# Optimization experiments

Hardware: AMD Instinct MI355X
Metric: run time of the kernel (lower is better)

Reference implementation:

```python
import jax, jax.numpy as jnp
import numpy as np

B, N, E, M, H = 2, 4096, 65536, 4, 256


def setup_inputs() -> dict:
    key = jax.random.key(0)
    ks = jax.random.split(key, 8)
    src = jax.random.randint(ks[0], (B, E), 0, N, dtype=jnp.int32)
    # targets: permutation of arange(E) % N per batch -> every node has >=1 incoming edge
    base = jnp.arange(E, dtype=jnp.int32) % N
    tgt = jnp.stack([jax.random.permutation(jax.random.fold_in(ks[1], b), base) for b in range(B)], axis=0)
    cfg_indices_padded = jnp.stack([src, tgt], axis=-1)  # [B, E, 2]
    hint_state = jax.random.normal(ks[2], (B, N, M, H), dtype=jnp.float32)
    node_fts = jax.random.normal(ks[3], (B, N, M, H), dtype=jnp.float32)
    edge_fts = jax.random.normal(ks[4], (B, E, H), dtype=jnp.float32)
    # hk.Linear default init scales
    edge_W = jax.random.truncated_normal(ks[5], -2.0, 2.0, (H, 1), dtype=jnp.float32) / np.sqrt(H)
    edge_b = jnp.zeros((1,), dtype=jnp.float32)
    update_W = jax.random.truncated_normal(ks[6], -2.0, 2.0, (H, H), dtype=jnp.float32) / np.sqrt(H)
    update_b = jnp.zeros((H,), dtype=jnp.float32)
    return {
        'cfg_indices_padded': cfg_indices_padded,
        'hint_state': hint_state,
        'node_fts': node_fts,
        'edge_fts': edge_fts,
        'edge_W': edge_W,
        'edge_b': edge_b,
        'update_W': update_W,
        'update_b': update_b,
    }


def reference(cfg_indices_padded, hint_state, node_fts, edge_fts, edge_W, edge_b, update_W, update_b):
    nb_nodes = node_fts.shape[1]
    src = cfg_indices_padded[..., 0]  # [B, E]
    tgt = cfg_indices_padded[..., 1]  # [B, E]
    # gather hint states at edge sources: [B, E, M, H]
    hint_sources = jnp.take_along_axis(hint_state, src[:, :, None, None], axis=1)
    # learned per-edge scalar coefficient: [B, E, 1]
    edge_coeff = edge_fts @ edge_W + edge_b
    hint_sources = edge_coeff[..., None] * hint_sources  # [B, E, M, H]
    # segment_max scatter-reduce per batch element -> [B, N, M, H]
    seg_max = jax.vmap(lambda d, s: jax.ops.segment_max(d, s, num_segments=nb_nodes))
    aggregated_hint = seg_max(hint_sources, tgt)
    # final linear update
    return (node_fts + aggregated_hint) @ update_W + update_b
```

## Files before the change

### kernel.cpp

```cpp
#include <hip/hip_runtime.h>

#define BB 2
#define NN 4096
#define EE 65536
#define MM 4
#define HH 256
#define NPB 16
#define NXCD 8
#define XPAD 264

typedef float vf4 __attribute__((ext_vector_type(4)));
typedef int vi2 __attribute__((ext_vector_type(2)));
typedef _Float16 vh4 __attribute__((ext_vector_type(4)));
typedef _Float16 f16x8 __attribute__((ext_vector_type(8)));
typedef float f32x4 __attribute__((ext_vector_type(4)));

#define PREP_A 2048
#define PREP_B 8192
#define PREP_C 64

__global__ __launch_bounds__(256) void k_prep(const float* __restrict__ edge_fts,
                                              const float* __restrict__ edge_W,
                                              const float* __restrict__ edge_b,
                                              const int* __restrict__ cfg,
                                              unsigned int* __restrict__ cnt,
                                              int2* __restrict__ packed,
                                              const float* __restrict__ hint,
                                              _Float16* __restrict__ h16,
                                              const float* __restrict__ W,
                                              _Float16* __restrict__ wt_hi) {
  const int blk = blockIdx.x;
  const int t = threadIdx.x;
  if (blk < PREP_A) {
    const int e0 = blk * 64 + (t >> 6) * 16;
    const int lane = t & 63;
    const float4 wv = *reinterpret_cast<const float4*>(edge_W + lane * 4);
    float s[16];
#pragma unroll
    for (int q = 0; q < 16; ++q) {
      const vf4 ef = __builtin_nontemporal_load(
          reinterpret_cast<const vf4*>(edge_fts + (size_t)(e0 + q) * HH + lane * 4));
      s[q] = ef.x * wv.x + ef.y * wv.y + ef.z * wv.z + ef.w * wv.w;
    }
#pragma unroll
    for (int off = 1; off < 64; off <<= 1) {
#pragma unroll
      for (int q = 0; q < 16; ++q) s[q] += __shfl_xor(s[q], off);
    }
    if (lane < 16) {
      float sv = s[15];
#pragma unroll
      for (int q = 14; q >= 0; --q) sv = (lane == q) ? s[q] : sv;
      const int widx = e0 + lane;
      const int b = widx >> 16;
      const vi2 st = __builtin_nontemporal_load(
          reinterpret_cast<const vi2*>(cfg + (size_t)widx * 2));
      const int slot = b * NN + st.y;
      const unsigned p = atomicAdd(&cnt[slot], 1u) & 15u;
      int2 v;
      v.x = st.x;
      v.y = __float_as_int(sv + edge_b[0]);
      packed[(size_t)slot * 16 + p] = v;
    }
  } else if (blk < PREP_A + PREP_B) {
    const int j = blk - PREP_A;
    const int unit = j & 7;
    const int g = j >> 3;
    const int b = unit >> 2;
    const int m = unit & 3;
    const int row = g * 4 + (t >> 6);
    const int c4 = t & 63;
    const size_t off = (((size_t)(b * NN + row) * MM + m) * HH) + c4 * 4;
    const vf4 v = __builtin_nontemporal_load(
        reinterpret_cast<const vf4*>(hint + off));
    vh4 h;
    h.x = (_Float16)v.x; h.y = (_Float16)v.y;
    h.z = (_Float16)v.z; h.w = (_Float16)v.w;
    *reinterpret_cast<vh4*>(h16 + off) = h;
  } else {
    const int jb = blk - PREP_A - PREP_B;
    const int j = jb * 4 + (t >> 6);
    const int h0 = (t & 63) * 4;
    vh4 hi;
    hi.x = (_Float16)W[(size_t)(h0 + 0) * HH + j];
    hi.y = (_Float16)W[(size_t)(h0 + 1) * HH + j];
    hi.z = (_Float16)W[(size_t)(h0 + 2) * HH + j];
    hi.w = (_Float16)W[(size_t)(h0 + 3) * HH + j];
    *reinterpret_cast<vh4*>(wt_hi + (size_t)j * HH + h0) = hi;
  }
}

__device__ __forceinline__ float4 fmax4(const float4& a, const float4& b) {
  return make_float4(fmaxf(a.x, b.x), fmaxf(a.y, b.y), fmaxf(a.z, b.z), fmaxf(a.w, b.w));
}

__device__ __forceinline__ float4 scmul(float c, const vh4& h) {
  return make_float4(c * (float)h.x, c * (float)h.y, c * (float)h.z, c * (float)h.w);
}

__global__ __launch_bounds__(256, 6) void k_fused(const _Float16* __restrict__ h16,
                                                  const float* __restrict__ node_fts,
                                                  const int2* __restrict__ packed,
                                                  const _Float16* __restrict__ wt_hi,
                                                  const float* __restrict__ bias,
                                                  float* __restrict__ out) {
  __shared__ _Float16 xs[NPB][XPAD];
  __shared__ int ssrc[NPB][16];
  __shared__ float scf[NPB][16];

  const int t = threadIdx.x;
  const int unit = blockIdx.x & (NXCD - 1);
  const int chunk = blockIdx.x >> 3;
  const int b = unit >> 2;
  const int m = unit & 3;
  const int n0 = chunk * NPB;
  const int w = t >> 6;
  const int lane = t & 63;
  const int r0 = w * 4;

  {
    const int i = t >> 4, k = t & 15;
    const int2 v = packed[(size_t)(b * NN + n0 + i) * 16 + k];
    ssrc[i][k] = v.x;
    scf[i][k] = __int_as_float(v.y);
  }

  const _Float16* hb = h16 + (size_t)b * NN * MM * HH + m * HH + lane * 4;

#pragma unroll 1
  for (int i = 0; i < 4; ++i) {
    const int lr = r0 + i;
    const int n = n0 + lr;
    vh4 hv[16];
#pragma unroll
    for (int k = 0; k < 16; ++k) {
      const int s = ssrc[lr][k];
      hv[k] = *reinterpret_cast<const vh4*>(hb + (size_t)s * (MM * HH));
    }
    float4 t8[8];
#pragma unroll
    for (int k = 0; k < 8; ++k)
      t8[k] = fmax4(scmul(scf[lr][2 * k], hv[2 * k]),
                    scmul(scf[lr][2 * k + 1], hv[2 * k + 1]));
#pragma unroll
    for (int k = 0; k < 4; ++k) t8[k] = fmax4(t8[k], t8[k + 4]);
    t8[0] = fmax4(t8[0], t8[2]);
    t8[1] = fmax4(t8[1], t8[3]);
    const float4 a = fmax4(t8[0], t8[1]);
    const vf4 nf = __builtin_nontemporal_load(reinterpret_cast<const vf4*>(
        node_fts + (((size_t)(b * NN + n) * MM + m) * HH) + lane * 4));
    vh4 xq;
    xq.x = (_Float16)(nf.x + a.x);
    xq.y = (_Float16)(nf.y + a.y);
    xq.z = (_Float16)(nf.z + a.z);
    xq.w = (_Float16)(nf.w + a.w);
    *reinterpret_cast<vh4*>(&xs[lr][lane * 4]) = xq;
  }
  __syncthreads();

  const int lr16 = lane & 15;
  const int kg = lane >> 4;

#pragma unroll 2
  for (int ct = 0; ct < 4; ++ct) {
    const int j = (w * 4 + ct) * 16 + lr16;
    const _Float16* bh = wt_hi + (size_t)j * HH + kg * 8;
    f32x4 acc = {0.f, 0.f, 0.f, 0.f};
#pragma unroll
    for (int kt = 0; kt < 8; ++kt) {
      const f16x8 bhi = *reinterpret_cast<const f16x8*>(bh + kt * 32);
      const f16x8 a = *reinterpret_cast<const f16x8*>(&xs[lr16][kt * 32 + kg * 8]);
      acc = __builtin_amdgcn_mfma_f32_16x16x32_f16(a, bhi, acc, 0, 0, 0);
    }
    const float bj = bias[j];
#pragma unroll
    for (int r = 0; r < 4; ++r) {
      const int n = n0 + kg * 4 + r;
      __builtin_nontemporal_store(
          acc[r] + bj, out + (((size_t)(b * NN + n) * MM + m) * HH) + j);
    }
  }
}

extern "C" void kernel_launch(void* const* d_in, const int* in_sizes, int n_in,
                              void* d_out, int out_size, void* d_ws, size_t ws_size,
                              hipStream_t stream) {
  const int* cfg = (const int*)d_in[0];
  const float* hint = (const float*)d_in[1];
  const float* node_fts = (const float*)d_in[2];
  const float* edge_fts = (const float*)d_in[3];
  const float* edge_W = (const float*)d_in[4];
  const float* edge_b = (const float*)d_in[5];
  const float* update_W = (const float*)d_in[6];
  const float* update_b = (const float*)d_in[7];
  float* out = (float*)d_out;

  char* ws = (char*)d_ws;
  unsigned int* cnt = (unsigned int*)ws;
  int2* packed = (int2*)(ws + 32768);
  _Float16* h16 = (_Float16*)(ws + 32768 + 1048576);
  _Float16* wt_hi = (_Float16*)(ws + 32768 + 1048576 + 16777216);

  k_prep<<<PREP_A + PREP_B + PREP_C, 256, 0, stream>>>(
      edge_fts, edge_W, edge_b, cfg, cnt, packed, hint, h16, update_W, wt_hi);
  k_fused<<<BB * MM * (NN / NPB), 256, 0, stream>>>(h16, node_fts, packed,
                                                    wt_hi, update_b, out);
}
```

Measured before the change: 92.64 us.

## Process two node chunks per block, overlapping gather of second with GEMM of first

Each block of the fused kernel now handles two 16-node chunks with double-buffered LDS tiles. While the MFMA GEMM for chunk A runs, the gather loads for chunk B are in flight, so memory latency is hidden behind matrix work. The grid is halved and launch bounds drop from 6 to 5 blocks per SIMD to allow more registers. The trade-off is fewer blocks in flight, which lowers occupancy and parallelism.

```diff
diff --git a/kernel.cpp b/kernel.cpp
--- a/kernel.cpp
+++ b/kernel.cpp
@@ -98,70 +98,109 @@
   return make_float4(c * (float)h.x, c * (float)h.y, c * (float)h.z, c * (float)h.w);
 }
 
-__global__ __launch_bounds__(256, 6) void k_fused(const _Float16* __restrict__ h16,
+__device__ __forceinline__ void consume_row(const vh4 hv[16], const float* scfrow,
+                                            const float* __restrict__ node_fts,
+                                            size_t nf_off, _Float16* xsrow, int lane) {
+  float4 t8[8];
+#pragma unroll
+  for (int k = 0; k < 8; ++k)
+    t8[k] = fmax4(scmul(scfrow[2 * k], hv[2 * k]),
+                  scmul(scfrow[2 * k + 1], hv[2 * k + 1]));
+#pragma unroll
+  for (int k = 0; k < 4; ++k) t8[k] = fmax4(t8[k], t8[k + 4]);
+  t8[0] = fmax4(t8[0], t8[2]);
+  t8[1] = fmax4(t8[1], t8[3]);
+  const float4 a = fmax4(t8[0], t8[1]);
+  const vf4 nf = __builtin_nontemporal_load(
+      reinterpret_cast<const vf4*>(node_fts + nf_off));
+  vh4 xq;
+  xq.x = (_Float16)(nf.x + a.x);
+  xq.y = (_Float16)(nf.y + a.y);
+  xq.z = (_Float16)(nf.z + a.z);
+  xq.w = (_Float16)(nf.w + a.w);
+  *reinterpret_cast<vh4*>(xsrow + lane * 4) = xq;
+}
+
+__global__ __launch_bounds__(256, 5) void k_fused(const _Float16* __restrict__ h16,
                                                   const float* __restrict__ node_fts,
                                                   const int2* __restrict__ packed,
                                                   const _Float16* __restrict__ wt_hi,
                                                   const float* __restrict__ bias,
                                                   float* __restrict__ out) {
-  __shared__ _Float16 xs[NPB][XPAD];
-  __shared__ int ssrc[NPB][16];
-  __shared__ float scf[NPB][16];
+  __shared__ _Float16 xsA[NPB][XPAD];
+  __shared__ _Float16 xsB[NPB][XPAD];
+  __shared__ int ssrc[2][NPB][16];
+  __shared__ float scf[2][NPB][16];
 
   const int t = threadIdx.x;
   const int unit = blockIdx.x & (NXCD - 1);
-  const int chunk = blockIdx.x >> 3;
+  const int cpair = blockIdx.x >> 3;
   const int b = unit >> 2;
   const int m = unit & 3;
-  const int n0 = chunk * NPB;
+  const int n0A = cpair * (2 * NPB);
+  const int n0B = n0A + NPB;
   const int w = t >> 6;
   const int lane = t & 63;
   const int r0 = w * 4;
+  const int lr16 = lane & 15;
+  const int kg = lane >> 4;
 
   {
     const int i = t >> 4, k = t & 15;
-    const int2 v = packed[(size_t)(b * NN + n0 + i) * 16 + k];
-    ssrc[i][k] = v.x;
-    scf[i][k] = __int_as_float(v.y);
+    const int2 vA = packed[(size_t)(b * NN + n0A + i) * 16 + k];
+    ssrc[0][i][k] = vA.x;
+    scf[0][i][k] = __int_as_float(vA.y);
+    const int2 vB = packed[(size_t)(b * NN + n0B + i) * 16 + k];
+    ssrc[1][i][k] = vB.x;
+    scf[1][i][k] = __int_as_float(vB.y);
   }
 
   const _Float16* hb = h16 + (size_t)b * NN * MM * HH + m * HH + lane * 4;
+  const size_t nfbase = ((size_t)b * NN * MM + m) * HH + lane * 4;
 
 #pragma unroll 1
   for (int i = 0; i < 4; ++i) {
     const int lr = r0 + i;
-    const int n = n0 + lr;
     vh4 hv[16];
 #pragma unroll
-    for (int k = 0; k < 16; ++k) {
-      const int s = ssrc[lr][k];
-      hv[k] = *reinterpret_cast<const vh4*>(hb + (size_t)s * (MM * HH));
-    }
-    float4 t8[8];
-#pragma unroll
-    for (int k = 0; k < 8; ++k)
-      t8[k] = fmax4(scmul(scf[lr][2 * k], hv[2 * k]),
-                    scmul(scf[lr][2 * k + 1], hv[2 * k + 1]));
-#pragma unroll
-    for (int k = 0; k < 4; ++k) t8[k] = fmax4(t8[k], t8[k + 4]);
-    t8[0] = fmax4(t8[0], t8[2]);
-    t8[1] = fmax4(t8[1], t8[3]);
-    const float4 a = fmax4(t8[0], t8[1]);
-    const vf4 nf = __builtin_nontemporal_load(reinterpret_cast<const vf4*>(
-        node_fts + (((size_t)(b * NN + n) * MM + m) * HH) + lane * 4));
-    vh4 xq;
-    xq.x = (_Float16)(nf.x + a.x);
-    xq.y = (_Float16)(nf.y + a.y);
-    xq.z = (_Float16)(nf.z + a.z);
-    xq.w = (_Float16)(nf.w + a.w);
-    *reinterpret_cast<vh4*>(&xs[lr][lane * 4]) = xq;
+    for (int k = 0; k < 16; ++k)
+      hv[k] = *reinterpret_cast<const vh4*>(hb + (size_t)ssrc[0][lr][k] * (MM * HH));
+    consume_row(hv, scf[0][lr], node_fts, nfbase + (size_t)(n0A + lr) * (MM * HH),
+                &xsA[lr][0], lane);
   }
   __syncthreads();
 
-  const int lr16 = lane & 15;
-  const int kg = lane >> 4;
-
-#pragma unroll 2
+#pragma unroll 1
+  for (int i = 0; i < 4; ++i) {
+    const int lr = r0 + i;
+    vh4 hv[16];
+#pragma unroll
+    for (int k = 0; k < 16; ++k)
+      hv[k] = *reinterpret_cast<const vh4*>(hb + (size_t)ssrc[1][lr][k] * (MM * HH));
+    {
+      const int j = (w * 4 + i) * 16 + lr16;
+      const _Float16* bh = wt_hi + (size_t)j * HH + kg * 8;
+      f32x4 acc = {0.f, 0.f, 0.f, 0.f};
+#pragma unroll
+      for (int kt = 0; kt < 8; ++kt) {
+        const f16x8 bhi = *reinterpret_cast<const f16x8*>(bh + kt * 32);
+        const f16x8 a = *reinterpret_cast<const f16x8*>(&xsA[lr16][kt * 32 + kg * 8]);
+        acc = __builtin_amdgcn_mfma_f32_16x16x32_f16(a, bhi, acc, 0, 0, 0);
+      }
+      const float bj = bias[j];
+#pragma unroll
+      for (int r = 0; r < 4; ++r) {
+        const int n = n0A + kg * 4 + r;
+        __builtin_nontemporal_store(
+            acc[r] + bj, out + (((size_t)(b * NN + n) * MM + m) * HH) + j);
+      }
+    }
+    consume_row(hv, scf[1][lr], node_fts, nfbase + (size_t)(n0B + lr) * (MM * HH),
+                &xsB[lr][0], lane);
+  }
+  __syncthreads();
+
+#pragma unroll 1
   for (int ct = 0; ct < 4; ++ct) {
     const int j = (w * 4 + ct) * 16 + lr16;
     const _Float16* bh = wt_hi + (size_t)j * HH + kg * 8;
@@ -169,13 +208,13 @@
 #pragma unroll
     for (int kt = 0; kt < 8; ++kt) {
       const f16x8 bhi = *reinterpret_cast<const f16x8*>(bh + kt * 32);
-      const f16x8 a = *reinterpret_cast<const f16x8*>(&xs[lr16][kt * 32 + kg * 8]);
+      const f16x8 a = *reinterpret_cast<const f16x8*>(&xsB[lr16][kt * 32 + kg * 8]);
       acc = __builtin_amdgcn_mfma_f32_16x16x32_f16(a, bhi, acc, 0, 0, 0);
     }
     const float bj = bias[j];
 #pragma unroll
     for (int r = 0; r < 4; ++r) {
-      const int n = n0 + kg * 4 + r;
+      const int n = n0B + kg * 4 + r;
       __builtin_nontemporal_store(
           acc[r] + bj, out + (((size_t)(b * NN + n) * MM + m) * HH) + j);
     }
@@ -203,6 +242,6 @@
 
   k_prep<<<PREP_A + PREP_B + PREP_C, 256, 0, stream>>>(
       edge_fts, edge_W, edge_b, cfg, cnt, packed, hint, h16, update_W, wt_hi);
-  k_fused<<<BB * MM * (NN / NPB), 256, 0, stream>>>(h16, node_fts, packed,
-                                                    wt_hi, update_b, out);
-}
+  k_fused<<<BB * MM * (NN / (2 * NPB)), 256, 0, stream>>>(h16, node_fts, packed,
+                                                          wt_hi, update_b, out);
+}
```

Result: slower. 108.1 us (+16.7%).
